# Kernel tuning notes

Hardware: AMD Instinct MI355X
Metric: run time of the kernel (lower is better)

## Reference

```python
import jax, jax.numpy as jnp
from jax import lax
import numpy as np

B, T, H = 128, 512, 512  # batch, seq_length, hidden_dim (== input_dim)


def _xavier(key, shape):
    fan_in, fan_out = shape[1], shape[0]
    limit = float(np.sqrt(6.0 / (fan_in + fan_out)))
    return jax.random.uniform(key, shape, jnp.float32, -limit, limit)


def setup_inputs() -> dict:
    key = jax.random.key(0)
    ks = jax.random.split(key, 10)
    s = 1.0 / np.sqrt(H)  # torch LSTM default init range
    return {
        "x": jax.random.normal(ks[0], (B, T, H), jnp.float32),
        "W_ih": jax.random.uniform(ks[1], (4 * H, H), jnp.float32, -s, s),
        "W_hh": jax.random.uniform(ks[2], (4 * H, H), jnp.float32, -s, s),
        "b_ih": jax.random.uniform(ks[3], (4 * H,), jnp.float32, -s, s),
        "b_hh": jax.random.uniform(ks[4], (4 * H,), jnp.float32, -s, s),
        "Ve": _xavier(ks[5], (1, H)),
        "U1": _xavier(ks[6], (H, 2 * H)),
        "U2": _xavier(ks[7], (H, H)),
        "W_out": _xavier(ks[8], (2, H)),
        "b_out": jnp.zeros((2,), jnp.float32),
    }


def _lstm(x, W_ih, W_hh, b_ih, b_hh):
    # x: [B, T, D] -> hidden states [B, T, H]; PyTorch gate order i,f,g,o
    b = b_ih + b_hh
    # precompute input projections for all timesteps: [T, B, 4H]
    xg = jnp.einsum('btd,gd->tbg', x, W_ih) + b

    def step(carry, xt):
        h, c = carry
        g = xt + h @ W_hh.T  # [B, 4H]
        i, f, gg, o = jnp.split(g, 4, axis=1)
        c = jax.nn.sigmoid(f) * c + jax.nn.sigmoid(i) * jnp.tanh(gg)
        h = jax.nn.sigmoid(o) * jnp.tanh(c)
        return (h, c), h

    h0 = jnp.zeros((x.shape[0], W_hh.shape[1]), x.dtype)
    (_, _), hs = lax.scan(step, (h0, h0), xg)
    return jnp.swapaxes(hs, 0, 1)  # [B, T, H]


def reference(x, W_ih, W_hh, b_ih, b_hh, Ve, U1, U2, W_out, b_out):
    h = _lstm(x, W_ih, W_hh, b_ih, b_hh)  # [B, T, H]
    h_last = h[:, -1, :]  # [B, H]
    # additive attention, vectorized over all timesteps
    Hdim = h.shape[-1]
    u1 = jnp.einsum('bth,gh->btg', h, U1[:, :Hdim]) + jnp.einsum('bh,gh->bg', h_last, U1[:, Hdim:])[:, None, :]
    u2 = jnp.einsum('btd,gd->btg', x, U2)
    u = jnp.tanh(u1 + u2)  # [B, T, H]
    e = jnp.einsum('bth,h->bt', u, Ve[0])
    alpha = jax.nn.softmax(e, axis=1)  # [B, T]
    context = jnp.einsum('bt,bth->bh', alpha, h)  # [B, H]
    params = context @ W_out.T + b_out  # [B, 2]
    mu = params[:, 0]
    sigma = jax.nn.softplus(params[:, 1]) + 1e-5
    return (mu, sigma)
```

## Files before the change

### kernel.cpp

```cpp
#include <hip/hip_runtime.h>
#include <stdint.h>


using short8  = __attribute__((ext_vector_type(8))) short;
using short4v = __attribute__((ext_vector_type(4))) short;
using floatx4 = __attribute__((ext_vector_type(4))) float;

#define MFMA16(a, b, c) __builtin_amdgcn_mfma_f32_16x16x32_bf16((a), (b), (c), 0, 0, 0)

__device__ __forceinline__ unsigned short f2b(float f) {
    unsigned u = __float_as_uint(f);
    u += 0x7FFFu + ((u >> 16) & 1u);
    return (unsigned short)(u >> 16);
}
__device__ __forceinline__ float b2f(unsigned short h) {
    return __uint_as_float(((unsigned)h) << 16);
}
__device__ __forceinline__ float sigm(float x) { return 1.0f / (1.0f + __expf(-x)); }
__device__ __forceinline__ float tanh_(float x) { return 1.0f - 2.0f / (__expf(2.0f * x) + 1.0f); }

__global__ __launch_bounds__(256) void prep(
    const float* __restrict__ x, const float* __restrict__ Wih, const float* __restrict__ Whh,
    const float* __restrict__ bih, const float* __restrict__ bhh,
    const float* __restrict__ U1, const float* __restrict__ U2,
    unsigned short* __restrict__ x_bf, unsigned short* __restrict__ Wih_bf,
    unsigned short* __restrict__ Whh_bf, unsigned short* __restrict__ U1a,
    unsigned short* __restrict__ U1b, unsigned short* __restrict__ U2b,
    float* __restrict__ bias)
{
    const long long NX4 = 33554432LL / 4;
    const long long NREST = 1048576LL + 1048576LL + 524288LL + 262144LL + 2048LL;
    const long long total = NX4 + NREST;
    for (long long u = (long long)blockIdx.x * 256 + threadIdx.x; u < total;
         u += (long long)gridDim.x * 256) {
        if (u < NX4) {
            float4 v = ((const float4*)x)[u];
            short4v o;
            o[0] = (short)f2b(v.x); o[1] = (short)f2b(v.y);
            o[2] = (short)f2b(v.z); o[3] = (short)f2b(v.w);
            *(short4v*)&x_bf[u * 4] = o;
        } else {
            long long i = u - NX4;
            if (i < 1048576) { Wih_bf[i] = f2b(Wih[i]); continue; }
            i -= 1048576;
            if (i < 1048576) { Whh_bf[i] = f2b(Whh[i]); continue; }
            i -= 1048576;
            if (i < 524288) {
                int row = (int)(i >> 10), col = (int)(i & 1023);
                if (col < 512) U1a[row * 512 + col] = f2b(U1[i]);
                else           U1b[row * 512 + (col - 512)] = f2b(U1[i]);
                continue;
            }
            i -= 524288;
            if (i < 262144) { U2b[i] = f2b(U2[i]); continue; }
            i -= 262144;
            bias[i] = bih[i] + bhh[i];
        }
    }
}

__global__ __launch_bounds__(256) void gemm_bt(
    const unsigned short* __restrict__ A, long long lda,
    const unsigned short* __restrict__ Bm, long long ldb,
    unsigned short* __restrict__ C, long long ldc,
    const float* __restrict__ bias, int mode)
{
    __shared__ __align__(16) unsigned short sbuf[2 * 128 * 72];
    unsigned short* At = sbuf;
    unsigned short* Bt = sbuf + 128 * 72;
    unsigned short* Ct = sbuf;

    const int m0 = blockIdx.x * 128, n0 = blockIdx.y * 128;
    const int tid = threadIdx.x;
    const int wv = tid >> 6, lane = tid & 63, l15 = lane & 15, q = lane >> 4;
    const int wm = wv & 1, wn = wv >> 1;

    floatx4 acc[4][4];
    for (int i = 0; i < 4; i++)
        for (int j = 0; j < 4; j++) acc[i][j] = (floatx4){0.f, 0.f, 0.f, 0.f};

    for (int k0 = 0; k0 < 512; k0 += 64) {
        for (int p = 0; p < 4; p++) {
            int idx = tid + p * 256;
            int row = idx >> 3, ch = idx & 7;
            *(short8*)&At[row * 72 + ch * 8] =
                *(const short8*)&A[(long long)(m0 + row) * lda + k0 + ch * 8];
            *(short8*)&Bt[row * 72 + ch * 8] =
                *(const short8*)&Bm[(long long)(n0 + row) * ldb + k0 + ch * 8];
        }
        __syncthreads();
        for (int ks = 0; ks < 64; ks += 32) {
            short8 af[4], bfv[4];
            for (int mi = 0; mi < 4; mi++)
                af[mi] = *(const short8*)&At[(wm * 64 + mi * 16 + l15) * 72 + ks + q * 8];
            for (int ni = 0; ni < 4; ni++)
                bfv[ni] = *(const short8*)&Bt[(wn * 64 + ni * 16 + l15) * 72 + ks + q * 8];
            for (int mi = 0; mi < 4; mi++)
                for (int ni = 0; ni < 4; ni++)
                    acc[mi][ni] = MFMA16(af[mi], bfv[ni], acc[mi][ni]);
        }
        __syncthreads();
    }

    float bv[4];
    for (int ni = 0; ni < 4; ni++)
        bv[ni] = bias ? bias[n0 + wn * 64 + ni * 16 + l15] : 0.0f;

    for (int mi = 0; mi < 4; mi++)
        for (int ni = 0; ni < 4; ni++)
            for (int r = 0; r < 4; r++)
                Ct[(wm * 64 + mi * 16 + q * 4 + r) * 128 + wn * 64 + ni * 16 + l15] =
                    f2b(acc[mi][ni][r] + bv[ni]);
    __syncthreads();

    const int tt0 = m0 & 511, bglob = m0 >> 9;
    for (int p = 0; p < 8; p++) {
        int idx = tid + p * 256;
        int row = idx >> 4, ch = idx & 15;
        if (mode) {
            int n = n0 + ch * 8;
            int gate = n >> 9, jg = (n >> 4) & 31, c0 = gate * 16 + (n & 15);
            long long dst = (((long long)(tt0 + row) * 32 + jg) * 128 + bglob) * 64 + c0;
            *(short8*)&C[dst] = *(const short8*)&Ct[row * 128 + ch * 8];
        } else {
            *(short8*)&C[(long long)(m0 + row) * ldc + n0 + ch * 8] =
                *(const short8*)&Ct[row * 128 + ch * 8];
        }
    }
}

__global__ __launch_bounds__(256) void lstm_rec(
    const unsigned short* __restrict__ xg,
    const unsigned short* __restrict__ Whh,
    unsigned short* __restrict__ h_all,
    unsigned long long* __restrict__ ring)
{
    __shared__ unsigned int At[2][16 * 264];

    const int tid = threadIdx.x;
    const int wv = tid >> 6, lane = tid & 63, l15 = lane & 15, q = lane >> 4;
    const int bg = blockIdx.x >> 5, jg = blockIdx.x & 31;
    const int b0 = bg * 16, hid0 = jg * 16;
    const int gate = l15 >> 2;
    const int hl = wv * 4 + (l15 & 3);
    const int hid = hid0 + hl;
    const long long jrow = (long long)gate * 512 + hid;

    short8 Wreg[16];
    for (int kk = 0; kk < 16; kk++)
        Wreg[kk] = *(const short8*)&Whh[jrow * 512 + kk * 32 + q * 8];

    unsigned long long* const rb0 = ring + (long long)b0 * 256;
    unsigned long long* const rb1 = ring + 32768 + (long long)b0 * 256;
    unsigned int* const ring32 = (unsigned int*)ring;

    float cst[4] = {0.f, 0.f, 0.f, 0.f};

    for (int t = 0; t < 512; t++) {
        const long long xbase =
            (((long long)t * 32 + jg) * 128 + b0) * 64 + gate * 16 + hl;
        float xv[4];
        #pragma unroll
        for (int r = 0; r < 4; r++)
            xv[r] = b2f(xg[xbase + (long long)(q * 4 + r) * 64]);

        floatx4 acc = (floatx4){0.f, 0.f, 0.f, 0.f};
        if (t > 0) {
            const unsigned want = (unsigned)(t - 1);
            unsigned long long* rb = ((t - 1) & 1) ? rb1 : rb0;
            unsigned long long w[16];
            #pragma unroll
            for (int i = 0; i < 16; i++)
                w[i] = __hip_atomic_load(&rb[tid + i * 256], __ATOMIC_RELAXED,
                                         __HIP_MEMORY_SCOPE_AGENT);
            while (true) {
                unsigned bad = 0;
                #pragma unroll
                for (int i = 0; i < 16; i++) {
                    unsigned lo = (unsigned)(w[i] >> 16) & 0xFFFFu;
                    unsigned hi = (unsigned)(w[i] >> 48);
                    bad |= (lo ^ want) | (hi ^ want);
                }
                if (!bad) break;
                #pragma unroll
                for (int i = 0; i < 16; i++) {
                    unsigned lo = (unsigned)(w[i] >> 16) & 0xFFFFu;
                    unsigned hi = (unsigned)(w[i] >> 48);
                    if ((lo ^ want) | (hi ^ want))
                        w[i] = __hip_atomic_load(&rb[tid + i * 256], __ATOMIC_RELAXED,
                                                 __HIP_MEMORY_SCOPE_AGENT);
                }
            }
            unsigned int* dst = &At[(t - 1) & 1][0];
            #pragma unroll
            for (int i = 0; i < 16; i++) {
                int idx = tid + i * 256;
                int row = idx >> 8, k = idx & 255;
                dst[row * 264 + k] =
                    (unsigned)(w[i] & 0xFFFFu) | ((unsigned)(w[i] >> 32) << 16);
            }
            __syncthreads();
            const unsigned int* ap = &At[(t - 1) & 1][l15 * 264 + q * 4];
            floatx4 a0 = (floatx4){0.f, 0.f, 0.f, 0.f};
            floatx4 a1 = (floatx4){0.f, 0.f, 0.f, 0.f};
            floatx4 a2 = (floatx4){0.f, 0.f, 0.f, 0.f};
            floatx4 a3 = (floatx4){0.f, 0.f, 0.f, 0.f};
            #pragma unroll
            for (int kk = 0; kk < 16; kk += 4) {
                a0 = MFMA16(*(const short8*)(ap + (kk + 0) * 16), Wreg[kk + 0], a0);
                a1 = MFMA16(*(const short8*)(ap + (kk + 1) * 16), Wreg[kk + 1], a1);
                a2 = MFMA16(*(const short8*)(ap + (kk + 2) * 16), Wreg[kk + 2], a2);
                a3 = MFMA16(*(const short8*)(ap + (kk + 3) * 16), Wreg[kk + 3], a3);
            }
            for (int r = 0; r < 4; r++) acc[r] = (a0[r] + a1[r]) + (a2[r] + a3[r]);
        }
        float p[4];
        #pragma unroll
        for (int r = 0; r < 4; r++) p[r] = acc[r] + xv[r];
        float vf[4], vg[4], vo[4];
        #pragma unroll
        for (int r = 0; r < 4; r++) vf[r] = __shfl_xor(p[r], 4);
        #pragma unroll
        for (int r = 0; r < 4; r++) vg[r] = __shfl_xor(p[r], 8);
        #pragma unroll
        for (int r = 0; r < 4; r++) vo[r] = __shfl_xor(p[r], 12);
        if (gate == 0) {
            #pragma unroll
            for (int r = 0; r < 4; r++) {
                float ig = sigm(p[r]);
                float fg = sigm(vf[r]);
                float gv = tanh_(vg[r]);
                float og = sigm(vo[r]);
                cst[r] = fg * cst[r] + ig * gv;
                float hv = og * tanh_(cst[r]);
                unsigned short hb = f2b(hv);
                const int b = b0 + q * 4 + r;
                __hip_atomic_store(&ring32[(t & 1) * 65536 + b * 512 + hid],
                                   ((unsigned)t << 16) | hb, __ATOMIC_RELAXED,
                                   __HIP_MEMORY_SCOPE_AGENT);
                h_all[(long long)b * 262144 + (long long)t * 512 + hid] = hb;
            }
        }
    }
}

__global__ __launch_bounds__(256) void attn_e(
    const unsigned short* __restrict__ h_all,
    const unsigned short* __restrict__ x_bf,
    const unsigned short* __restrict__ U1a, const unsigned short* __restrict__ U2b,
    const unsigned short* __restrict__ u1b,
    const float* __restrict__ Ve,
    float* __restrict__ e)
{
    __shared__ __align__(16) unsigned short Bt[512 * 40];
    __shared__ __align__(16) unsigned short At[32 * 40];
    __shared__ float ered[4][32];

    const int tid = threadIdx.x;
    const int wv = tid >> 6, lane = tid & 63, l15 = lane & 15, q = lane >> 4;
    const int b = blockIdx.x >> 4, t0 = (blockIdx.x & 15) * 32;

    floatx4 acc[2][8];
    for (int mi = 0; mi < 2; mi++)
        for (int ni = 0; ni < 8; ni++) acc[mi][ni] = (floatx4){0.f, 0.f, 0.f, 0.f};

    for (int it = 0; it < 32; it++) {
        const int phase = it >> 4, kk = (it & 15) * 32;
        const unsigned short* Asrc = phase ? x_bf : h_all;
        const unsigned short* Bsrc = phase ? U2b : U1a;
        __syncthreads();
        for (int idx = tid; idx < 2048; idx += 256) {
            int row = idx >> 2, ch = idx & 3;
            *(short8*)&Bt[row * 40 + ch * 8] =
                *(const short8*)&Bsrc[(long long)row * 512 + kk + ch * 8];
        }
        if (tid < 128) {
            int row = tid >> 2, ch = tid & 3;
            *(short8*)&At[row * 40 + ch * 8] =
                *(const short8*)&Asrc[(long long)(b * 512 + t0 + row) * 512 + kk + ch * 8];
        }
        __syncthreads();
        short8 af[2];
        for (int mi = 0; mi < 2; mi++)
            af[mi] = *(const short8*)&At[(mi * 16 + l15) * 40 + q * 8];
        for (int ni = 0; ni < 8; ni++) {
            short8 bfv = *(const short8*)&Bt[(wv * 128 + ni * 16 + l15) * 40 + q * 8];
            acc[0][ni] = MFMA16(af[0], bfv, acc[0][ni]);
            acc[1][ni] = MFMA16(af[1], bfv, acc[1][ni]);
        }
    }

    float s[2][4] = {{0.f, 0.f, 0.f, 0.f}, {0.f, 0.f, 0.f, 0.f}};
    for (int ni = 0; ni < 8; ni++) {
        int n = wv * 128 + ni * 16 + l15;
        float ub = b2f(u1b[b * 512 + n]);
        float vev = Ve[n];
        for (int mi = 0; mi < 2; mi++)
            for (int r = 0; r < 4; r++)
                s[mi][r] += vev * tanh_(acc[mi][ni][r] + ub);
    }
    for (int off = 1; off <= 8; off <<= 1)
        for (int mi = 0; mi < 2; mi++)
            for (int r = 0; r < 4; r++) s[mi][r] += __shfl_xor(s[mi][r], off);
    if (l15 == 0)
        for (int mi = 0; mi < 2; mi++)
            for (int r = 0; r < 4; r++) ered[wv][mi * 16 + q * 4 + r] = s[mi][r];
    __syncthreads();
    if (tid < 32)
        e[(long long)b * 512 + t0 + tid] =
            ered[0][tid] + ered[1][tid] + ered[2][tid] + ered[3][tid];
}

__global__ __launch_bounds__(256) void attn_out(
    const float* __restrict__ e, const unsigned short* __restrict__ h_all,
    const float* __restrict__ Wout, const float* __restrict__ bout,
    float* __restrict__ outp)
{
    __shared__ float sm[512];
    __shared__ float red[8];
    const int b = blockIdx.x, tid = threadIdx.x;
    const int wv = tid >> 6, lane = tid & 63;

    float e0 = e[b * 512 + tid], e1 = e[b * 512 + 256 + tid];
    float mx = fmaxf(e0, e1);
    for (int off = 32; off; off >>= 1) mx = fmaxf(mx, __shfl_xor(mx, off));
    if (lane == 0) red[wv] = mx;
    __syncthreads();
    mx = fmaxf(fmaxf(red[0], red[1]), fmaxf(red[2], red[3]));

    float s0 = __expf(e0 - mx), s1 = __expf(e1 - mx);
    sm[tid] = s0; sm[256 + tid] = s1;
    float ss = s0 + s1;
    for (int off = 32; off; off >>= 1) ss += __shfl_xor(ss, off);
    if (lane == 0) red[4 + wv] = ss;
    __syncthreads();
    float inv = 1.0f / (red[4] + red[5] + red[6] + red[7]);

    const long long base = (long long)b * 262144;
    float a0 = 0.f, a1 = 0.f;
    for (int t = 0; t < 512; t++) {
        float al = sm[t];
        a0 += al * b2f(h_all[base + t * 512 + tid]);
        a1 += al * b2f(h_all[base + t * 512 + 256 + tid]);
    }
    a0 *= inv; a1 *= inv;

    float q0 = a0 * Wout[tid] + a1 * Wout[256 + tid];
    float q1 = a0 * Wout[512 + tid] + a1 * Wout[768 + tid];
    for (int off = 32; off; off >>= 1) { q0 += __shfl_xor(q0, off); q1 += __shfl_xor(q1, off); }
    __syncthreads();
    if (lane == 0) { red[wv] = q0; red[4 + wv] = q1; }
    __syncthreads();
    if (tid == 0) {
        float P0 = red[0] + red[1] + red[2] + red[3] + bout[0];
        float P1 = red[4] + red[5] + red[6] + red[7] + bout[1];
        outp[b] = P0;
        float sp = (P1 > 15.0f) ? P1 : log1pf(__expf(P1));
        outp[128 + b] = sp + 1e-5f;
    }
}

extern "C" void kernel_launch(void* const* d_in, const int* in_sizes, int n_in,
                              void* d_out, int out_size, void* d_ws, size_t ws_size,
                              hipStream_t stream)
{
    const float* x    = (const float*)d_in[0];
    const float* Wih  = (const float*)d_in[1];
    const float* Whh  = (const float*)d_in[2];
    const float* bih  = (const float*)d_in[3];
    const float* bhh  = (const float*)d_in[4];
    const float* Ve   = (const float*)d_in[5];
    const float* U1   = (const float*)d_in[6];
    const float* U2   = (const float*)d_in[7];
    const float* Wout = (const float*)d_in[8];
    const float* bout = (const float*)d_in[9];
    float* out = (float*)d_out;

    char* ws = (char*)d_ws;
    size_t off = 0;
    auto alloc = [&](size_t bytes) -> void* {
        void* p = ws + off;
        off += (bytes + 255) & ~(size_t)255;
        return p;
    };
    unsigned short* x_bf   = (unsigned short*)alloc(33554432ull * 2);
    unsigned short* Wih_bf = (unsigned short*)alloc(1048576ull * 2);
    unsigned short* Whh_bf = (unsigned short*)alloc(1048576ull * 2);
    unsigned short* U1a    = (unsigned short*)alloc(262144ull * 2);
    unsigned short* U1b    = (unsigned short*)alloc(262144ull * 2);
    unsigned short* U2b    = (unsigned short*)alloc(262144ull * 2);
    float*          bias   = (float*)alloc(2048ull * 4);
    unsigned short* xg     = (unsigned short*)alloc(134217728ull * 2);
    unsigned short* h_all  = (unsigned short*)alloc(33554432ull * 2);
    unsigned short* u1bv   = (unsigned short*)alloc(65536ull * 2);
    float*          e      = (float*)alloc(65536ull * 4);
    unsigned long long* ring = (unsigned long long*)alloc(65536ull * 8);
    if (off > ws_size) return;

    prep<<<4096, 256, 0, stream>>>(x, Wih, Whh, bih, bhh, U1, U2,
                                   x_bf, Wih_bf, Whh_bf, U1a, U1b, U2b, bias);
    gemm_bt<<<dim3(512, 16), 256, 0, stream>>>(x_bf, 512, Wih_bf, 512,
                                               xg, 2048, bias, 1);
    lstm_rec<<<256, 256, 0, stream>>>(xg, Whh_bf, h_all, ring);
    gemm_bt<<<dim3(1, 4), 256, 0, stream>>>(h_all + 511 * 512, 262144, U1b, 512,
                                            u1bv, 512, nullptr, 0);
    attn_e<<<2048, 256, 0, stream>>>(h_all, x_bf, U1a, U2b, u1bv, Ve, e);
    attn_out<<<128, 256, 0, stream>>>(e, h_all, Wout, bout, out);
}
```

Baseline: 3.065 ms.

## Replace per-element tagged h ring with packed data plus per-wave ready flags

The recurrent LSTM kernel used to tag every bf16 hidden value with its timestep inside 64-bit ring words, and every consumer polled all of its data words. Now the bf16 pairs are packed into 32-bit ring words with no tag. Each wave publishes one timestep flag after an s_waitcnt vmcnt(0), and consumers spin on a single 8-byte flag load per lane before reading the data once. This halves the ring traffic and makes the spin-wait lighter. In exchange, correctness now depends on the data stores becoming visible before the relaxed flag store, with no explicit release/acquire ordering.

```diff
diff --git a/kernel.cpp b/kernel.cpp
--- a/kernel.cpp
+++ b/kernel.cpp
@@ -129,13 +129,16 @@
     }
 }
 
+#define NBG 8
+#define NJG 32
 __global__ __launch_bounds__(256) void lstm_rec(
     const unsigned short* __restrict__ xg,
     const unsigned short* __restrict__ Whh,
     unsigned short* __restrict__ h_all,
-    unsigned long long* __restrict__ ring)
-{
-    __shared__ unsigned int At[2][16 * 264];
+    unsigned int* __restrict__ ring,
+    int* __restrict__ sent)
+{
+    __shared__ __align__(16) unsigned int At[2][16 * 264];
 
     const int tid = threadIdx.x;
     const int wv = tid >> 6, lane = tid & 63, l15 = lane & 15, q = lane >> 4;
@@ -150,10 +153,6 @@
     for (int kk = 0; kk < 16; kk++)
         Wreg[kk] = *(const short8*)&Whh[jrow * 512 + kk * 32 + q * 8];
 
-    unsigned long long* const rb0 = ring + (long long)b0 * 256;
-    unsigned long long* const rb1 = ring + 32768 + (long long)b0 * 256;
-    unsigned int* const ring32 = (unsigned int*)ring;
-
     float cst[4] = {0.f, 0.f, 0.f, 0.f};
 
     for (int t = 0; t < 512; t++) {
@@ -167,40 +166,31 @@
         floatx4 acc = (floatx4){0.f, 0.f, 0.f, 0.f};
         if (t > 0) {
             const unsigned want = (unsigned)(t - 1);
-            unsigned long long* rb = ((t - 1) & 1) ? rb1 : rb0;
-            unsigned long long w[16];
+            const int sl = (t - 1) & 1;
+            const unsigned long long* sp = (const unsigned long long*)
+                &sent[sl * (NBG * 128) + bg * 128 + lane * 2];
+            while (true) {
+                unsigned long long sv = __hip_atomic_load(sp, __ATOMIC_RELAXED,
+                                                          __HIP_MEMORY_SCOPE_AGENT);
+                bool ok = ((unsigned)(sv & 0xFFFFFFFFull) == want) &&
+                          ((unsigned)(sv >> 32) == want);
+                if (__all(ok)) break;
+            }
+            const unsigned long long* rb = (const unsigned long long*)
+                (ring + sl * 32768 + b0 * 256);
+            unsigned long long d[8];
             #pragma unroll
-            for (int i = 0; i < 16; i++)
-                w[i] = __hip_atomic_load(&rb[tid + i * 256], __ATOMIC_RELAXED,
+            for (int i = 0; i < 8; i++)
+                d[i] = __hip_atomic_load(&rb[i * 256 + tid], __ATOMIC_RELAXED,
                                          __HIP_MEMORY_SCOPE_AGENT);
-            while (true) {
-                unsigned bad = 0;
-                #pragma unroll
-                for (int i = 0; i < 16; i++) {
-                    unsigned lo = (unsigned)(w[i] >> 16) & 0xFFFFu;
-                    unsigned hi = (unsigned)(w[i] >> 48);
-                    bad |= (lo ^ want) | (hi ^ want);
-                }
-                if (!bad) break;
-                #pragma unroll
-                for (int i = 0; i < 16; i++) {
-                    unsigned lo = (unsigned)(w[i] >> 16) & 0xFFFFu;
-                    unsigned hi = (unsigned)(w[i] >> 48);
-                    if ((lo ^ want) | (hi ^ want))
-                        w[i] = __hip_atomic_load(&rb[tid + i * 256], __ATOMIC_RELAXED,
-                                                 __HIP_MEMORY_SCOPE_AGENT);
-                }
-            }
-            unsigned int* dst = &At[(t - 1) & 1][0];
             #pragma unroll
-            for (int i = 0; i < 16; i++) {
-                int idx = tid + i * 256;
-                int row = idx >> 8, k = idx & 255;
-                dst[row * 264 + k] =
-                    (unsigned)(w[i] & 0xFFFFu) | ((unsigned)(w[i] >> 32) << 16);
+            for (int i = 0; i < 8; i++) {
+                int widx = i * 512 + tid * 2;
+                int row = widx >> 8, k = widx & 255;
+                *(unsigned long long*)&At[sl][row * 264 + k] = d[i];
             }
             __syncthreads();
-            const unsigned int* ap = &At[(t - 1) & 1][l15 * 264 + q * 4];
+            const unsigned int* ap = &At[sl][l15 * 264 + q * 4];
             floatx4 a0 = (floatx4){0.f, 0.f, 0.f, 0.f};
             floatx4 a1 = (floatx4){0.f, 0.f, 0.f, 0.f};
             floatx4 a2 = (floatx4){0.f, 0.f, 0.f, 0.f};
@@ -235,12 +225,20 @@
                 float hv = og * tanh_(cst[r]);
                 unsigned short hb = f2b(hv);
                 const int b = b0 + q * 4 + r;
-                __hip_atomic_store(&ring32[(t & 1) * 65536 + b * 512 + hid],
-                                   ((unsigned)t << 16) | hb, __ATOMIC_RELAXED,
-                                   __HIP_MEMORY_SCOPE_AGENT);
                 h_all[(long long)b * 262144 + (long long)t * 512 + hid] = hb;
+                unsigned partner = (unsigned)__shfl_xor((int)hb, 1);
+                if ((l15 & 1) == 0) {
+                    unsigned word = (unsigned)hb | (partner << 16);
+                    __hip_atomic_store(&ring[(t & 1) * 32768 + b * 256 + (hid >> 1)],
+                                       word, __ATOMIC_RELAXED,
+                                       __HIP_MEMORY_SCOPE_AGENT);
+                }
             }
         }
+        asm volatile("s_waitcnt vmcnt(0)" ::: "memory");
+        if (lane == 0)
+            __hip_atomic_store(&sent[(t & 1) * (NBG * 128) + bg * 128 + jg * 4 + wv],
+                               t, __ATOMIC_RELAXED, __HIP_MEMORY_SCOPE_AGENT);
     }
 }
 
@@ -394,14 +392,15 @@
     unsigned short* h_all  = (unsigned short*)alloc(33554432ull * 2);
     unsigned short* u1bv   = (unsigned short*)alloc(65536ull * 2);
     float*          e      = (float*)alloc(65536ull * 4);
-    unsigned long long* ring = (unsigned long long*)alloc(65536ull * 8);
+    unsigned int*   ring   = (unsigned int*)alloc(65536ull * 4);
+    int*            sentf  = (int*)alloc(2048ull * 4);
     if (off > ws_size) return;
 
     prep<<<4096, 256, 0, stream>>>(x, Wih, Whh, bih, bhh, U1, U2,
                                    x_bf, Wih_bf, Whh_bf, U1a, U1b, U2b, bias);
     gemm_bt<<<dim3(512, 16), 256, 0, stream>>>(x_bf, 512, Wih_bf, 512,
                                                xg, 2048, bias, 1);
-    lstm_rec<<<256, 256, 0, stream>>>(xg, Whh_bf, h_all, ring);
+    lstm_rec<<<256, 256, 0, stream>>>(xg, Whh_bf, h_all, ring, sentf);
     gemm_bt<<<dim3(1, 4), 256, 0, stream>>>(h_all + 511 * 512, 262144, U1b, 512,
                                             u1bv, 512, nullptr, 0);
     attn_e<<<2048, 256, 0, stream>>>(h_all, x_bf, U1a, U2b, u1bv, Ve, e);
```

After: 3.796 ms. 1.24x slower.

## Process two batch groups per LSTM recurrence block and halve the grid

Applied to the files above, without the earlier changes.

Each recurrence block now handles two 16-row batch groups, pair and pair+4, one after the other within each timestep, so the grid drops from 256 to 128 blocks. Cell state is kept per group, and the ring buffer is addressed as 32-bit words with a per-group base. The aim is to cut the number of blocks spinning on the global ring and to let the second group's wait overlap with the first group's compute. In exchange, each block does twice the serial MFMA and gate work per step, which can lengthen the per-step critical path.

```diff
diff --git a/kernel.cpp b/kernel.cpp
--- a/kernel.cpp
+++ b/kernel.cpp
@@ -133,112 +133,116 @@
     const unsigned short* __restrict__ xg,
     const unsigned short* __restrict__ Whh,
     unsigned short* __restrict__ h_all,
-    unsigned long long* __restrict__ ring)
+    unsigned int* __restrict__ ring)
 {
     __shared__ unsigned int At[2][16 * 264];
 
     const int tid = threadIdx.x;
     const int wv = tid >> 6, lane = tid & 63, l15 = lane & 15, q = lane >> 4;
-    const int bg = blockIdx.x >> 5, jg = blockIdx.x & 31;
-    const int b0 = bg * 16, hid0 = jg * 16;
+    const int pair = blockIdx.x >> 5, jg = blockIdx.x & 31;
     const int gate = l15 >> 2;
     const int hl = wv * 4 + (l15 & 3);
-    const int hid = hid0 + hl;
+    const int hid = jg * 16 + hl;
     const long long jrow = (long long)gate * 512 + hid;
 
     short8 Wreg[16];
     for (int kk = 0; kk < 16; kk++)
         Wreg[kk] = *(const short8*)&Whh[jrow * 512 + kk * 32 + q * 8];
 
-    unsigned long long* const rb0 = ring + (long long)b0 * 256;
-    unsigned long long* const rb1 = ring + 32768 + (long long)b0 * 256;
-    unsigned int* const ring32 = (unsigned int*)ring;
-
-    float cst[4] = {0.f, 0.f, 0.f, 0.f};
+    float cst[2][4] = {{0.f, 0.f, 0.f, 0.f}, {0.f, 0.f, 0.f, 0.f}};
 
     for (int t = 0; t < 512; t++) {
-        const long long xbase =
-            (((long long)t * 32 + jg) * 128 + b0) * 64 + gate * 16 + hl;
-        float xv[4];
+        float xv[2][4];
         #pragma unroll
-        for (int r = 0; r < 4; r++)
-            xv[r] = b2f(xg[xbase + (long long)(q * 4 + r) * 64]);
-
-        floatx4 acc = (floatx4){0.f, 0.f, 0.f, 0.f};
-        if (t > 0) {
-            const unsigned want = (unsigned)(t - 1);
-            unsigned long long* rb = ((t - 1) & 1) ? rb1 : rb0;
-            unsigned long long w[16];
+        for (int hf = 0; hf < 2; hf++) {
+            const int b0 = (pair + hf * 4) * 16;
+            const long long xbase =
+                (((long long)t * 32 + jg) * 128 + b0) * 64 + gate * 16 + hl;
             #pragma unroll
-            for (int i = 0; i < 16; i++)
-                w[i] = __hip_atomic_load(&rb[tid + i * 256], __ATOMIC_RELAXED,
-                                         __HIP_MEMORY_SCOPE_AGENT);
-            while (true) {
-                unsigned bad = 0;
+            for (int r = 0; r < 4; r++)
+                xv[hf][r] = b2f(xg[xbase + (long long)(q * 4 + r) * 64]);
+        }
+
+        #pragma unroll
+        for (int hf = 0; hf < 2; hf++) {
+            const int b0 = (pair + hf * 4) * 16;
+            floatx4 acc = (floatx4){0.f, 0.f, 0.f, 0.f};
+            if (t > 0) {
+                const unsigned want = (unsigned)(t - 1);
+                unsigned long long* rb = (unsigned long long*)
+                    (ring + ((t - 1) & 1) * 65536 + b0 * 512);
+                unsigned long long w[16];
+                #pragma unroll
+                for (int i = 0; i < 16; i++)
+                    w[i] = __hip_atomic_load(&rb[tid + i * 256], __ATOMIC_RELAXED,
+                                             __HIP_MEMORY_SCOPE_AGENT);
+                while (true) {
+                    unsigned bad = 0;
+                    #pragma unroll
+                    for (int i = 0; i < 16; i++) {
+                        unsigned lo = (unsigned)(w[i] >> 16) & 0xFFFFu;
+                        unsigned hi = (unsigned)(w[i] >> 48);
+                        bad |= (lo ^ want) | (hi ^ want);
+                    }
+                    if (!bad) break;
+                    #pragma unroll
+                    for (int i = 0; i < 16; i++) {
+                        unsigned lo = (unsigned)(w[i] >> 16) & 0xFFFFu;
+                        unsigned hi = (unsigned)(w[i] >> 48);
+                        if ((lo ^ want) | (hi ^ want))
+                            w[i] = __hip_atomic_load(&rb[tid + i * 256], __ATOMIC_RELAXED,
+                                                     __HIP_MEMORY_SCOPE_AGENT);
+                    }
+                }
+                unsigned int* dst = &At[hf][0];
                 #pragma unroll
                 for (int i = 0; i < 16; i++) {
-                    unsigned lo = (unsigned)(w[i] >> 16) & 0xFFFFu;
-                    unsigned hi = (unsigned)(w[i] >> 48);
-                    bad |= (lo ^ want) | (hi ^ want);
+                    int idx = tid + i * 256;
+                    int row = idx >> 8, k = idx & 255;
+                    dst[row * 264 + k] =
+                        (unsigned)(w[i] & 0xFFFFu) | ((unsigned)(w[i] >> 32) << 16);
                 }
-                if (!bad) break;
+                __syncthreads();
+                const unsigned int* ap = &At[hf][l15 * 264 + q * 4];
+                floatx4 a0 = (floatx4){0.f, 0.f, 0.f, 0.f};
+                floatx4 a1 = (floatx4){0.f, 0.f, 0.f, 0.f};
+                floatx4 a2 = (floatx4){0.f, 0.f, 0.f, 0.f};
+                floatx4 a3 = (floatx4){0.f, 0.f, 0.f, 0.f};
                 #pragma unroll
-                for (int i = 0; i < 16; i++) {
-                    unsigned lo = (unsigned)(w[i] >> 16) & 0xFFFFu;
-                    unsigned hi = (unsigned)(w[i] >> 48);
-                    if ((lo ^ want) | (hi ^ want))
-                        w[i] = __hip_atomic_load(&rb[tid + i * 256], __ATOMIC_RELAXED,
-                                                 __HIP_MEMORY_SCOPE_AGENT);
+                for (int kk = 0; kk < 16; kk += 4) {
+                    a0 = MFMA16(*(const short8*)(ap + (kk + 0) * 16), Wreg[kk + 0], a0);
+                    a1 = MFMA16(*(const short8*)(ap + (kk + 1) * 16), Wreg[kk + 1], a1);
+                    a2 = MFMA16(*(const short8*)(ap + (kk + 2) * 16), Wreg[kk + 2], a2);
+                    a3 = MFMA16(*(const short8*)(ap + (kk + 3) * 16), Wreg[kk + 3], a3);
                 }
+                for (int r = 0; r < 4; r++) acc[r] = (a0[r] + a1[r]) + (a2[r] + a3[r]);
             }
-            unsigned int* dst = &At[(t - 1) & 1][0];
+            float p[4];
             #pragma unroll
-            for (int i = 0; i < 16; i++) {
-                int idx = tid + i * 256;
-                int row = idx >> 8, k = idx & 255;
-                dst[row * 264 + k] =
-                    (unsigned)(w[i] & 0xFFFFu) | ((unsigned)(w[i] >> 32) << 16);
-            }
-            __syncthreads();
-            const unsigned int* ap = &At[(t - 1) & 1][l15 * 264 + q * 4];
-            floatx4 a0 = (floatx4){0.f, 0.f, 0.f, 0.f};
-            floatx4 a1 = (floatx4){0.f, 0.f, 0.f, 0.f};
-            floatx4 a2 = (floatx4){0.f, 0.f, 0.f, 0.f};
-            floatx4 a3 = (floatx4){0.f, 0.f, 0.f, 0.f};
+            for (int r = 0; r < 4; r++) p[r] = acc[r] + xv[hf][r];
+            float vf[4], vg[4], vo[4];
             #pragma unroll
-            for (int kk = 0; kk < 16; kk += 4) {
-                a0 = MFMA16(*(const short8*)(ap + (kk + 0) * 16), Wreg[kk + 0], a0);
-                a1 = MFMA16(*(const short8*)(ap + (kk + 1) * 16), Wreg[kk + 1], a1);
-                a2 = MFMA16(*(const short8*)(ap + (kk + 2) * 16), Wreg[kk + 2], a2);
-                a3 = MFMA16(*(const short8*)(ap + (kk + 3) * 16), Wreg[kk + 3], a3);
-            }
-            for (int r = 0; r < 4; r++) acc[r] = (a0[r] + a1[r]) + (a2[r] + a3[r]);
-        }
-        float p[4];
-        #pragma unroll
-        for (int r = 0; r < 4; r++) p[r] = acc[r] + xv[r];
-        float vf[4], vg[4], vo[4];
-        #pragma unroll
-        for (int r = 0; r < 4; r++) vf[r] = __shfl_xor(p[r], 4);
-        #pragma unroll
-        for (int r = 0; r < 4; r++) vg[r] = __shfl_xor(p[r], 8);
-        #pragma unroll
-        for (int r = 0; r < 4; r++) vo[r] = __shfl_xor(p[r], 12);
-        if (gate == 0) {
+            for (int r = 0; r < 4; r++) vf[r] = __shfl_xor(p[r], 4);
             #pragma unroll
-            for (int r = 0; r < 4; r++) {
-                float ig = sigm(p[r]);
-                float fg = sigm(vf[r]);
-                float gv = tanh_(vg[r]);
-                float og = sigm(vo[r]);
-                cst[r] = fg * cst[r] + ig * gv;
-                float hv = og * tanh_(cst[r]);
-                unsigned short hb = f2b(hv);
-                const int b = b0 + q * 4 + r;
-                __hip_atomic_store(&ring32[(t & 1) * 65536 + b * 512 + hid],
-                                   ((unsigned)t << 16) | hb, __ATOMIC_RELAXED,
-                                   __HIP_MEMORY_SCOPE_AGENT);
-                h_all[(long long)b * 262144 + (long long)t * 512 + hid] = hb;
+            for (int r = 0; r < 4; r++) vg[r] = __shfl_xor(p[r], 8);
+            #pragma unroll
+            for (int r = 0; r < 4; r++) vo[r] = __shfl_xor(p[r], 12);
+            if (gate == 0) {
+                #pragma unroll
+                for (int r = 0; r < 4; r++) {
+                    float ig = sigm(p[r]);
+                    float fg = sigm(vf[r]);
+                    float gv = tanh_(vg[r]);
+                    float og = sigm(vo[r]);
+                    cst[hf][r] = fg * cst[hf][r] + ig * gv;
+                    float hv = og * tanh_(cst[hf][r]);
+                    unsigned short hb = f2b(hv);
+                    const int b = b0 + q * 4 + r;
+                    __hip_atomic_store(&ring[(t & 1) * 65536 + b * 512 + hid],
+                                       ((unsigned)t << 16) | hb, __ATOMIC_RELAXED,
+                                       __HIP_MEMORY_SCOPE_AGENT);
+                    h_all[(long long)b * 262144 + (long long)t * 512 + hid] = hb;
+                }
             }
         }
     }
@@ -394,14 +398,14 @@
     unsigned short* h_all  = (unsigned short*)alloc(33554432ull * 2);
     unsigned short* u1bv   = (unsigned short*)alloc(65536ull * 2);
     float*          e      = (float*)alloc(65536ull * 4);
-    unsigned long long* ring = (unsigned long long*)alloc(65536ull * 8);
+    unsigned int*   ring   = (unsigned int*)alloc(131072ull * 4);
     if (off > ws_size) return;
 
     prep<<<4096, 256, 0, stream>>>(x, Wih, Whh, bih, bhh, U1, U2,
                                    x_bf, Wih_bf, Whh_bf, U1a, U1b, U2b, bias);
     gemm_bt<<<dim3(512, 16), 256, 0, stream>>>(x_bf, 512, Wih_bf, 512,
                                                xg, 2048, bias, 1);
-    lstm_rec<<<256, 256, 0, stream>>>(xg, Whh_bf, h_all, ring);
+    lstm_rec<<<128, 256, 0, stream>>>(xg, Whh_bf, h_all, ring);
     gemm_bt<<<dim3(1, 4), 256, 0, stream>>>(h_all + 511 * 512, 262144, U1b, 512,
                                             u1bv, 512, nullptr, 0);
     attn_e<<<2048, 256, 0, stream>>>(h_all, x_bf, U1a, U2b, u1bv, Ve, e);
```

After: 3.645 ms. 1.19x slower.
